# Performance work log

Hardware: AMD Instinct MI355X
Metric: run time of the kernel (lower is better)

The kernel has to match this reference:

```python
import jax, jax.numpy as jnp
import numpy as np

EPS = 2.220446049250313e-16  # sys.float_info.epsilon
TEMP = 0.01

def maxpool2(x):
    b, c, h, w = x.shape
    return x.reshape(b, c, h // 2, 2, w // 2, 2).max(axis=(3, 5))

def conv1x1(x, w, b):
    # x: [B,C,H,W], w: [O,C], b: [O]
    return jnp.einsum('bchw,oc->bohw', x, w) + b[None, :, None, None]

def unfold3(x):
    # F.unfold(kernel_size=3, padding=1) -> [B, C*9, H*W], channel-major ordering
    b, c, h, w = x.shape
    xp = jnp.pad(x, ((0, 0), (0, 0), (1, 1), (1, 1)))
    patches = jnp.stack([xp[:, :, i:i + h, j:j + w] for i in range(3) for j in range(3)], axis=2)  # [b,c,9,h,w]
    return patches.reshape(b, c * 9, h * w)

def center_norm(t):
    # mean-center and L2-normalize over the patch-feature dim (dim=1)
    t = t - t.mean(axis=1, keepdims=True)
    return t / (jnp.linalg.norm(t, axis=1, keepdims=True) + EPS)

def setup_inputs() -> dict:
    key = jax.random.key(0)
    ks = jax.random.split(key, 12)
    B, C, H, W = 4, 256, 64, 64
    inp = {
        'block_fea': jax.random.normal(ks[0], (B, C, H, W), jnp.float32),
        'spp_input': jax.random.normal(ks[1], (B, C, H, W), jnp.float32),
        'click_map': jax.random.uniform(ks[2], (B, 2, H * 8, W * 8), jnp.float32),
        # click feature pyramid convs (1x1)
        'w1': jax.random.normal(ks[3], (64, 2), jnp.float32) * 0.1,
        'b1': jnp.zeros((64,), jnp.float32),
        'w2': jax.random.normal(ks[4], (128, 64), jnp.float32) * 0.05,
        'b2': jnp.zeros((128,), jnp.float32),
        'w3': jax.random.normal(ks[5], (256, 128), jnp.float32) * 0.05,
        'b3': jnp.zeros((256,), jnp.float32),
        # final cat conv: 512 -> 256
        'wc': jax.random.normal(ks[6], (256, 512), jnp.float32) * 0.03,
        'bc': jnp.zeros((256,), jnp.float32),
    }
    return inp

def reference(block_fea, spp_input, click_map, w1, b1, w2, b2, w3, b3, wc, bc):
    B, C, H, W = block_fea.shape
    HW = H * W
    # click feature: MaxPool-Conv x3 (2ch -> 64 -> 128 -> 256), spatial /8
    cf = conv1x1(maxpool2(click_map), w1, b1)
    cf = conv1x1(maxpool2(cf), w2, b2)
    cf = conv1x1(maxpool2(cf), w3, b3)  # [B,256,H,W]
    # get_corre: unfold + mean-center + L2-normalize (cosine similarity over 3x3 patches)
    theta = center_norm(unfold3(block_fea))  # [B, C*9, HW]
    # spp_input is already (H,W): bilinear interpolate to same size is identity
    phi = center_norm(unfold3(spp_input))    # [B, C*9, HW]
    f = jnp.einsum('bcm,bcn->bmn', theta, phi) / TEMP  # [B, HW, HW]
    f_div_C = jax.nn.softmax(f, axis=-1)
    # propagate: click_fea already (H,W) -> identity interpolate
    ref = cf.reshape(B, C, HW)
    y = jnp.einsum('bmn,bcn->bcm', f_div_C, ref).reshape(B, C, H, W)
    # upsample to (H,W) is identity; concat + 1x1 conv
    out = conv1x1(jnp.concatenate([block_fea, y], axis=1), wc, bc)
    return out
```

## Files before the change

kernel.cpp:

```cpp
#include <hip/hip_runtime.h>
#include <math.h>

#define EPSF 2.220446049250313e-16f

typedef short bf16x8 __attribute__((ext_vector_type(8)));
typedef float f32x4 __attribute__((ext_vector_type(4)));

static __device__ __forceinline__ unsigned short f2bf(float x) {
  union { float f; unsigned u; } v; v.f = x;
  unsigned r = v.u + 0x7fffu + ((v.u >> 16) & 1u);
  return (unsigned short)(r >> 16);
}

__global__ __launch_bounds__(256) void k_zero(float* __restrict__ p) {
  const int t = blockIdx.x * 256 + threadIdx.x;
  float4 z = make_float4(0.f, 0.f, 0.f, 0.f);
  *reinterpret_cast<float4*>(&p[(size_t)t * 4]) = z;
}

__global__ __launch_bounds__(256) void k_tcast(const float* __restrict__ src0,
    unsigned short* __restrict__ dst0, int R, int C,
    size_t src_z, size_t dst_z, float* __restrict__ SA, float* __restrict__ QA) {
  __shared__ float ld[64][65];
  const float* src = src0 + blockIdx.z * src_z;
  unsigned short* dst = dst0 + blockIdx.z * dst_z;
  const int c0 = blockIdx.x * 64, r0 = blockIdx.y * 64;
  const int t = threadIdx.x;
  const int colr = t & 63, rowr = t >> 6;
  float s = 0.f, q = 0.f;
  #pragma unroll
  for (int i = 0; i < 16; ++i) {
    const int rl = rowr + i * 4;
    const float v = src[(size_t)(r0 + rl) * C + c0 + colr];
    ld[colr][rl] = v;
    s += v; q += v * v;
  }
  if (SA) {
    atomicAdd(&SA[blockIdx.z * 4096 + c0 + colr], s);
    atomicAdd(&QA[blockIdx.z * 4096 + c0 + colr], q);
  }
  __syncthreads();
  const int rl = t & 63, clb = t >> 6;
  #pragma unroll
  for (int i = 0; i < 16; ++i) {
    const int cl = clb + i * 4;
    dst[(size_t)(c0 + cl) * R + r0 + rl] = f2bf(ld[cl][rl]);
  }
}

__global__ __launch_bounds__(128) void k_pyr1(const float* __restrict__ click,
    const float* __restrict__ w1, const float* __restrict__ b1,
    const float* __restrict__ w2, const float* __restrict__ b2,
    float* __restrict__ cf2) {
  __shared__ float pool1[16][8];
  __shared__ float pooled64[16][64];
  const int b = blockIdx.y;
  const int pg = blockIdx.x;
  const int tid = threadIdx.x;
  {
    const int q = tid >> 3, s = (tid >> 1) & 3, c = tid & 1;
    const int p2 = pg * 16 + q;
    const int y2 = p2 >> 7, x2 = p2 & 127;
    const int sy = s >> 1, sx = s & 1;
    const int row = 4 * y2 + 2 * sy, col = 4 * x2 + 2 * sx;
    const float* base = click + (((size_t)(b * 2 + c)) * 512 + row) * 512 + col;
    pool1[q][s * 2 + c] = fmaxf(fmaxf(base[0], base[1]), fmaxf(base[512], base[513]));
  }
  __syncthreads();
  {
    const int c1 = tid & 63, qh = tid >> 6;
    const float wa = w1[c1 * 2], wb = w1[c1 * 2 + 1], bb = b1[c1];
    #pragma unroll
    for (int r = 0; r < 8; ++r) {
      const int q = qh * 8 + r;
      float v = -3.4e38f;
      #pragma unroll
      for (int s = 0; s < 4; ++s)
        v = fmaxf(v, bb + wa * pool1[q][s * 2] + wb * pool1[q][s * 2 + 1]);
      pooled64[q][c1] = v;
    }
  }
  __syncthreads();
  float acc[16];
  #pragma unroll
  for (int q = 0; q < 16; ++q) acc[q] = b2[tid];
  const float4* wrow = reinterpret_cast<const float4*>(w2 + tid * 64);
  #pragma unroll
  for (int k4 = 0; k4 < 16; ++k4) {
    const float4 w = wrow[k4];
    #pragma unroll
    for (int q = 0; q < 16; ++q) {
      const float4 p = *reinterpret_cast<const float4*>(&pooled64[q][k4 * 4]);
      acc[q] += w.x * p.x + w.y * p.y + w.z * p.z + w.w * p.w;
    }
  }
  #pragma unroll
  for (int q = 0; q < 16; ++q)
    cf2[((size_t)b * 16384 + pg * 16 + q) * 128 + tid] = acc[q];
}

__global__ __launch_bounds__(256) void k_pyr2(const float* __restrict__ cf2,
    const float* __restrict__ w3, const float* __restrict__ b3,
    float* __restrict__ cf3) {
  __shared__ float pooled[16][128];
  const int b = blockIdx.y;
  const int pb = blockIdx.x;
  const int tid = threadIdx.x;
  #pragma unroll
  for (int i = 0; i < 8; ++i) {
    const int idx = tid + 256 * i;
    const int q = idx >> 7, c = idx & 127;
    const int p = pb * 16 + q;
    const int y = p >> 6, x = p & 63;
    const size_t r0 = (size_t)b * 16384 + (2 * y) * 128 + 2 * x;
    const float* s0 = cf2 + r0 * 128 + c;
    pooled[q][c] = fmaxf(fmaxf(s0[0], s0[128]), fmaxf(s0[128 * 128], s0[128 * 129]));
  }
  __syncthreads();
  float acc[16];
  #pragma unroll
  for (int q = 0; q < 16; ++q) acc[q] = b3[tid];
  const float4* wrow = reinterpret_cast<const float4*>(w3 + tid * 128);
  #pragma unroll
  for (int k4 = 0; k4 < 32; ++k4) {
    const float4 w = wrow[k4];
    #pragma unroll
    for (int q = 0; q < 16; ++q) {
      const float4 p = *reinterpret_cast<const float4*>(&pooled[q][k4 * 4]);
      acc[q] += w.x * p.x + w.y * p.y + w.z * p.z + w.w * p.w;
    }
  }
  #pragma unroll
  for (int q = 0; q < 16; ++q)
    cf3[((size_t)b * 4096 + pb * 16 + q) * 256 + tid] = acc[q];
}

__global__ __launch_bounds__(256) void k_stats9(const float* __restrict__ SA,
    const float* __restrict__ QA, const float* __restrict__ SB, const float* __restrict__ QB,
    float* __restrict__ muA, float* __restrict__ invA,
    float* __restrict__ muB, float* __restrict__ invB) {
  const int b = blockIdx.y;
  const int m = blockIdx.x * 256 + threadIdx.x;
  const int y = m >> 6, x = m & 63;
  const int base = b * 4096;
  float sa = 0, qa = 0, sb = 0, qb = 0;
  #pragma unroll
  for (int dy = -1; dy <= 1; ++dy) {
    const int yy = y + dy;
    if ((unsigned)yy >= 64u) continue;
    #pragma unroll
    for (int dx = -1; dx <= 1; ++dx) {
      const int xx = x + dx;
      if ((unsigned)xx >= 64u) continue;
      const int idx = base + yy * 64 + xx;
      sa += SA[idx]; qa += QA[idx];
      sb += SB[idx]; qb += QB[idx];
    }
  }
  const float ma = sa * (1.f / 2304.f);
  const float mb = sb * (1.f / 2304.f);
  const float na = sqrtf(fmaxf(qa - 2304.f * ma * ma, 0.f));
  const float nb = sqrtf(fmaxf(qb - 2304.f * mb * mb, 0.f));
  muA[base + m] = ma;
  invA[base + m] = 1.f / (na + EPSF);
  muB[base + m] = mb;
  invB[base + m] = 1.f / (nb + EPSF);
}

#define ROWP 40
static __device__ __forceinline__ void stage_tile(const unsigned short* __restrict__ src,
    size_t srow, int r0, int k0, unsigned short* __restrict__ lds, int tid) {
  #pragma unroll
  for (int p = 0; p < 2; ++p) {
    const int idx = tid + p * 256;
    const int m = idx >> 2, q = idx & 3;
    const bf16x8 v = *reinterpret_cast<const bf16x8*>(src + (size_t)(r0 + m) * srow + k0 + q * 8);
    *reinterpret_cast<bf16x8*>(lds + m * ROWP + q * 8) = v;
  }
}

static __device__ __forceinline__ bf16x8 frag(const unsigned short* __restrict__ lds,
                                              int row, int q) {
  return *reinterpret_cast<const bf16x8*>(lds + row * ROWP + q * 8);
}

__global__ __launch_bounds__(256) void k_gemm_g(const unsigned short* __restrict__ At,
    const unsigned short* __restrict__ Bt, float* __restrict__ G) {
  __shared__ unsigned short As[128 * ROWP];
  __shared__ unsigned short Bs[128 * ROWP];
  const int tid = threadIdx.x;
  const int lin = blockIdx.y * 32 + blockIdx.x;
  const int nlin = ((lin & 7) << 7) | (lin >> 3);
  const int m0 = (nlin >> 5) * 128, n0 = (nlin & 31) * 128;
  const int l = tid & 63, w = tid >> 6;
  const int wr = w >> 1, wc = w & 1;
  const int q = l >> 4, lr = l & 15;
  f32x4 acc[4][4];
  #pragma unroll
  for (int i = 0; i < 4; ++i)
    #pragma unroll
    for (int j = 0; j < 4; ++j)
      acc[i][j] = f32x4{0.f, 0.f, 0.f, 0.f};
  for (int k0 = 0; k0 < 256; k0 += 32) {
    stage_tile(At, 256, m0, k0, As, tid);
    stage_tile(Bt, 256, n0, k0, Bs, tid);
    __syncthreads();
    bf16x8 a[4], bvv[4];
    #pragma unroll
    for (int i = 0; i < 4; ++i) a[i] = frag(As, wr * 64 + i * 16 + lr, q);
    #pragma unroll
    for (int j = 0; j < 4; ++j) bvv[j] = frag(Bs, wc * 64 + j * 16 + lr, q);
    #pragma unroll
    for (int i = 0; i < 4; ++i)
      #pragma unroll
      for (int j = 0; j < 4; ++j)
        acc[i][j] = __builtin_amdgcn_mfma_f32_16x16x32_bf16(a[i], bvv[j], acc[i][j], 0, 0, 0);
    __syncthreads();
  }
  const int rb = 4 * q;
  #pragma unroll
  for (int i = 0; i < 4; ++i)
    #pragma unroll
    for (int j = 0; j < 4; ++j) {
      const size_t base = (size_t)(m0 + wr * 64 + i * 16 + rb) * 4096 + n0 + wc * 64 + j * 16 + lr;
      #pragma unroll
      for (int r = 0; r < 4; ++r)
        G[base + (size_t)r * 4096] = acc[i][j][r];
    }
}

__global__ __launch_bounds__(256) void k_fsoft(const float* __restrict__ G,
    const float* __restrict__ muA, const float* __restrict__ invA,
    const float* __restrict__ muB, const float* __restrict__ invB,
    unsigned short* __restrict__ P) {
  __shared__ float redm[4];
  __shared__ float reds[4];
  const int m = ((blockIdx.x & 7) << 9) | (blockIdx.x >> 3);
  const int tid = threadIdx.x;
  const int ym = m >> 6, xm = m & 63;
  const int xn = tid & 63, ty = tid >> 6;

  const float* base[9];
  bool xok[9];
  #pragma unroll
  for (int dy = -1; dy <= 1; ++dy) {
    #pragma unroll
    for (int dx = -1; dx <= 1; ++dx) {
      const int g = (dy + 1) * 3 + (dx + 1);
      const bool rv = ((unsigned)(ym + dy) < 64u) && ((unsigned)(xm + dx) < 64u);
      const int d = dy * 64 + dx;
      base[g] = rv ? (G + (size_t)(m + d) * 4096 + d) : G;
      xok[g] = rv && ((unsigned)(xn + dx) < 64u);
    }
  }

  float acc[16];
  #pragma unroll
  for (int u = 0; u < 16; ++u) acc[u] = 0.f;

  #pragma unroll
  for (int uc = 0; uc < 4; ++uc) {
    float v[36];
    #pragma unroll
    for (int g = 0; g < 9; ++g) {
      #pragma unroll
      for (int r = 0; r < 4; ++r) {
        const int u = uc * 4 + r;
        v[g * 4 + r] = base[g][u * 256 + tid];
      }
    }
    #pragma unroll
    for (int g = 0; g < 9; ++g) {
      const int dy = g / 3 - 1;
      #pragma unroll
      for (int r = 0; r < 4; ++r) {
        const int u = uc * 4 + r;
        const bool ok = xok[g] && ((unsigned)(4 * u + ty + dy) < 64u);
        acc[u] += ok ? v[g * 4 + r] : 0.f;
      }
    }
  }

  const float s1 = 2304.f * muA[m];
  const float ia100 = invA[m] * 100.f;
  float mx = -3.4e38f;
  #pragma unroll
  for (int u = 0; u < 16; ++u) {
    const int n = tid + u * 256;
    const float lg = (acc[u] - s1 * muB[n]) * (ia100 * invB[n]);
    acc[u] = lg;
    mx = fmaxf(mx, lg);
  }
  #pragma unroll
  for (int off = 32; off; off >>= 1) mx = fmaxf(mx, __shfl_xor(mx, off));
  const int wave = tid >> 6, lane = tid & 63;
  if (lane == 0) redm[wave] = mx;
  __syncthreads();
  mx = fmaxf(fmaxf(redm[0], redm[1]), fmaxf(redm[2], redm[3]));
  float s = 0.f;
  #pragma unroll
  for (int u = 0; u < 16; ++u) {
    acc[u] = __expf(acc[u] - mx);
    s += acc[u];
  }
  #pragma unroll
  for (int off = 32; off; off >>= 1) s += __shfl_xor(s, off);
  if (lane == 0) reds[wave] = s;
  __syncthreads();
  s = reds[0] + reds[1] + reds[2] + reds[3];
  const float inv = 1.f / s;
  unsigned short* row = P + (size_t)m * 4096;
  #pragma unroll
  for (int u = 0; u < 16; ++u)
    row[tid + u * 256] = f2bf(acc[u] * inv);
}

__global__ __launch_bounds__(256) void k_pv(const unsigned short* __restrict__ CFt,
    const unsigned short* __restrict__ P, float* __restrict__ Y) {
  __shared__ unsigned short As[128 * ROWP];
  __shared__ unsigned short Bs[128 * ROWP];
  const int tid = threadIdx.x;
  const int c0 = blockIdx.y * 128, mb0 = blockIdx.x * 128;
  const int kbase = blockIdx.z * 512;
  const int l = tid & 63, w = tid >> 6;
  const int wr = w >> 1, wc = w & 1;
  const int q = l >> 4, lr = l & 15;
  f32x4 acc[4][4];
  #pragma unroll
  for (int i = 0; i < 4; ++i)
    #pragma unroll
    for (int j = 0; j < 4; ++j)
      acc[i][j] = f32x4{0.f, 0.f, 0.f, 0.f};
  for (int ks = 0; ks < 512; ks += 32) {
    const int k0 = kbase + ks;
    stage_tile(CFt, 4096, c0, k0, As, tid);
    stage_tile(P, 4096, mb0, k0, Bs, tid);
    __syncthreads();
    bf16x8 a[4], bvv[4];
    #pragma unroll
    for (int i = 0; i < 4; ++i) a[i] = frag(As, wr * 64 + i * 16 + lr, q);
    #pragma unroll
    for (int j = 0; j < 4; ++j) bvv[j] = frag(Bs, wc * 64 + j * 16 + lr, q);
    #pragma unroll
    for (int i = 0; i < 4; ++i)
      #pragma unroll
      for (int j = 0; j < 4; ++j)
        acc[i][j] = __builtin_amdgcn_mfma_f32_16x16x32_bf16(a[i], bvv[j], acc[i][j], 0, 0, 0);
    __syncthreads();
  }
  const int rb = 4 * q;
  #pragma unroll
  for (int i = 0; i < 4; ++i)
    #pragma unroll
    for (int j = 0; j < 4; ++j) {
      #pragma unroll
      for (int r = 0; r < 4; ++r) {
        const size_t o = (size_t)(c0 + wr * 64 + i * 16 + rb + r) * 4096 + mb0 + wc * 64 + j * 16 + lr;
        atomicAdd(&Y[o], acc[i][j][r]);
      }
    }
}

__global__ __launch_bounds__(256) void k_final(const float* __restrict__ WC,
    const float* __restrict__ bc, const float* __restrict__ BF,
    const float* __restrict__ Y, float* __restrict__ OUT) {
  __shared__ float As[16][68];
  __shared__ float Bs[16][64];
  const int b = blockIdx.z;
  const int tid = threadIdx.x;
  const int tx = tid & 15, ty = tid >> 4;
  const int o0 = blockIdx.y * 64, m0 = blockIdx.x * 64;
  float acc[4][4] = {};
  for (int k0 = 0; k0 < 512; k0 += 16) {
    #pragma unroll
    for (int t = 0; t < 4; ++t) {
      const int e = tid + t * 256;
      const int oo = e >> 4, kk = e & 15;
      As[kk][oo] = WC[(size_t)(o0 + oo) * 512 + k0 + kk];
    }
    #pragma unroll
    for (int t = 0; t < 4; ++t) {
      const int e = tid + t * 256;
      const int kk = e >> 6, col = e & 63;
      const int k = k0 + kk;
      const float* src = (k < 256)
          ? (BF + ((size_t)(b * 256 + k)) * 4096)
          : (Y + ((size_t)(b * 256 + (k - 256))) * 4096);
      Bs[kk][col] = src[m0 + col];
    }
    __syncthreads();
    #pragma unroll
    for (int k = 0; k < 16; ++k) {
      const float4 a4 = *reinterpret_cast<const float4*>(&As[k][ty * 4]);
      const float4 b4 = *reinterpret_cast<const float4*>(&Bs[k][tx * 4]);
      const float av[4] = {a4.x, a4.y, a4.z, a4.w};
      const float bv[4] = {b4.x, b4.y, b4.z, b4.w};
      #pragma unroll
      for (int i = 0; i < 4; ++i)
        #pragma unroll
        for (int j = 0; j < 4; ++j)
          acc[i][j] += av[i] * bv[j];
    }
    __syncthreads();
  }
  #pragma unroll
  for (int i = 0; i < 4; ++i) {
    const int o = o0 + ty * 4 + i;
    const float bias = bc[o];
    float4 v = make_float4(acc[i][0] + bias, acc[i][1] + bias,
                           acc[i][2] + bias, acc[i][3] + bias);
    *reinterpret_cast<float4*>(&OUT[((size_t)(b * 256 + o)) * 4096 + m0 + tx * 4]) = v;
  }
}

extern "C" void kernel_launch(void* const* d_in, const int* in_sizes, int n_in,
                              void* d_out, int out_size, void* d_ws, size_t ws_size,
                              hipStream_t stream) {
  const float* block_fea = (const float*)d_in[0];
  const float* spp       = (const float*)d_in[1];
  const float* click     = (const float*)d_in[2];
  const float* w1 = (const float*)d_in[3];
  const float* b1 = (const float*)d_in[4];
  const float* w2 = (const float*)d_in[5];
  const float* b2 = (const float*)d_in[6];
  const float* w3 = (const float*)d_in[7];
  const float* b3 = (const float*)d_in[8];
  const float* wc = (const float*)d_in[9];
  const float* bc = (const float*)d_in[10];
  float* out = (float*)d_out;

  float* ws = (float*)d_ws;
  const size_t M1 = 1024 * 1024;
  float* cf2  = ws;
  float* G    = ws + 256;
  unsigned short* Pb  = (unsigned short*)(ws + 17 * M1);
  unsigned short* At  = (unsigned short*)(ws + 25 * M1);
  unsigned short* Bt  = (unsigned short*)(ws + 27 * M1);
  unsigned short* CFt = (unsigned short*)(ws + 29 * M1);
  float* cf3  = ws + 31 * M1;
  float* Y    = ws + 35 * M1;
  float* SA   = ws + 39 * M1;
  float* QA   = SA + 16384;
  float* SB   = QA + 16384;
  float* QB   = SB + 16384;
  float* muA  = QB + 16384;
  float* invA = muA + 16384;
  float* muB  = invA + 16384;
  float* invB = muB + 16384;

  k_zero<<<dim3(4160), 256, 0, stream>>>(Y);
  k_pyr1<<<dim3(1024, 4), 128, 0, stream>>>(click, w1, b1, w2, b2, cf2);
  k_pyr2<<<dim3(256, 4), 256, 0, stream>>>(cf2, w3, b3, cf3);
  k_tcast<<<dim3(64, 4, 4), 256, 0, stream>>>(block_fea, At, 256, 4096,
                                              (size_t)256 * 4096, (size_t)4096 * 256, SA, QA);
  k_tcast<<<dim3(64, 4, 4), 256, 0, stream>>>(spp, Bt, 256, 4096,
                                              (size_t)256 * 4096, (size_t)4096 * 256, SB, QB);
  k_tcast<<<dim3(4, 64, 4), 256, 0, stream>>>(cf3, CFt, 4096, 256,
                                              (size_t)4096 * 256, (size_t)256 * 4096,
                                              (float*)nullptr, (float*)nullptr);
  k_stats9<<<dim3(16, 4), 256, 0, stream>>>(SA, QA, SB, QB, muA, invA, muB, invB);

  for (int b = 0; b < 4; ++b) {
    const unsigned short* Atb = At + (size_t)b * 4096 * 256;
    const unsigned short* Btb = Bt + (size_t)b * 4096 * 256;
    k_gemm_g<<<dim3(32, 32), 256, 0, stream>>>(Atb, Btb, G);
    k_fsoft<<<dim3(4096), 256, 0, stream>>>(G, muA + b * 4096, invA + b * 4096,
                                            muB + b * 4096, invB + b * 4096, Pb);
    k_pv<<<dim3(32, 2, 8), 256, 0, stream>>>(CFt + (size_t)b * 256 * 4096, Pb,
                                             Y + (size_t)b * 256 * 4096);
  }

  k_final<<<dim3(64, 4, 4), 256, 0, stream>>>(wc, bc, block_fea, Y, out);
}
```

Before: 625.1 us.

## Reassociate the final conv into the propagation GEMM and drop the fp32 final kernel

The final 1x1 conv is split over the concatenated input. The block_fea half becomes a bf16 MFMA GEMM that writes bias-initialised output. The click-feature half is applied to cf3 before propagation, so k_pv atomically accumulates straight into the output. This removes the scalar fp32 k_final GEMM, the large Y zeroing and the cf3 transpose, adding two small MFMA GEMMs and a weight split/cast kernel. The trade-off is extra bf16 rounding on block_fea, the weights and the pre-multiplied click features.

Result: faster. 574.8 us (-8.1%).

```diff
diff --git a/kernel.cpp b/kernel.cpp
--- a/kernel.cpp
+++ b/kernel.cpp
@@ -16,6 +16,15 @@
   const int t = blockIdx.x * 256 + threadIdx.x;
   float4 z = make_float4(0.f, 0.f, 0.f, 0.f);
   *reinterpret_cast<float4*>(&p[(size_t)t * 4]) = z;
+}
+
+__global__ __launch_bounds__(256) void k_wsplit(const float* __restrict__ wc,
+    unsigned short* __restrict__ wcLb, unsigned short* __restrict__ wcRb) {
+  const int idx = blockIdx.x * 256 + threadIdx.x;
+  const int o = idx >> 9, k = idx & 511;
+  const float v = wc[idx];
+  if (k < 256) wcLb[o * 256 + k] = f2bf(v);
+  else         wcRb[o * 256 + (k - 256)] = f2bf(v);
 }
 
 __global__ __launch_bounds__(256) void k_tcast(const float* __restrict__ src0,
@@ -101,7 +110,7 @@
 
 __global__ __launch_bounds__(256) void k_pyr2(const float* __restrict__ cf2,
     const float* __restrict__ w3, const float* __restrict__ b3,
-    float* __restrict__ cf3) {
+    unsigned short* __restrict__ cf3b) {
   __shared__ float pooled[16][128];
   const int b = blockIdx.y;
   const int pb = blockIdx.x;
@@ -132,7 +141,7 @@
   }
   #pragma unroll
   for (int q = 0; q < 16; ++q)
-    cf3[((size_t)b * 4096 + pb * 16 + q) * 256 + tid] = acc[q];
+    cf3b[((size_t)b * 4096 + pb * 16 + q) * 256 + tid] = f2bf(acc[q]);
 }
 
 __global__ __launch_bounds__(256) void k_stats9(const float* __restrict__ SA,
@@ -229,6 +238,100 @@
     }
 }
 
+__global__ __launch_bounds__(256) void k_gemm_cf2(const unsigned short* __restrict__ wcRb,
+    const unsigned short* __restrict__ cf3b, unsigned short* __restrict__ CF2t) {
+  __shared__ unsigned short As[128 * ROWP];
+  __shared__ unsigned short Bs[128 * ROWP];
+  const int b = blockIdx.z;
+  const int tid = threadIdx.x;
+  const int o0 = blockIdx.y * 128, n0 = blockIdx.x * 128;
+  const unsigned short* Bb = cf3b + (size_t)b * 4096 * 256;
+  unsigned short* outb = CF2t + (size_t)b * 256 * 4096;
+  const int l = tid & 63, w = tid >> 6;
+  const int wr = w >> 1, wcol = w & 1;
+  const int q = l >> 4, lr = l & 15;
+  f32x4 acc[4][4];
+  #pragma unroll
+  for (int i = 0; i < 4; ++i)
+    #pragma unroll
+    for (int j = 0; j < 4; ++j)
+      acc[i][j] = f32x4{0.f, 0.f, 0.f, 0.f};
+  for (int k0 = 0; k0 < 256; k0 += 32) {
+    stage_tile(wcRb, 256, o0, k0, As, tid);
+    stage_tile(Bb, 256, n0, k0, Bs, tid);
+    __syncthreads();
+    bf16x8 a[4], bvv[4];
+    #pragma unroll
+    for (int i = 0; i < 4; ++i) a[i] = frag(As, wr * 64 + i * 16 + lr, q);
+    #pragma unroll
+    for (int j = 0; j < 4; ++j) bvv[j] = frag(Bs, wcol * 64 + j * 16 + lr, q);
+    #pragma unroll
+    for (int i = 0; i < 4; ++i)
+      #pragma unroll
+      for (int j = 0; j < 4; ++j)
+        acc[i][j] = __builtin_amdgcn_mfma_f32_16x16x32_bf16(a[i], bvv[j], acc[i][j], 0, 0, 0);
+    __syncthreads();
+  }
+  const int rb = 4 * q;
+  #pragma unroll
+  for (int i = 0; i < 4; ++i)
+    #pragma unroll
+    for (int j = 0; j < 4; ++j) {
+      const size_t base = (size_t)(o0 + wr * 64 + i * 16 + rb) * 4096 + n0 + wcol * 64 + j * 16 + lr;
+      #pragma unroll
+      for (int r = 0; r < 4; ++r)
+        outb[base + (size_t)r * 4096] = f2bf(acc[i][j][r]);
+    }
+}
+
+__global__ __launch_bounds__(256) void k_gemm_oinit(const unsigned short* __restrict__ wcLb,
+    const unsigned short* __restrict__ At, const float* __restrict__ bc,
+    float* __restrict__ OUT) {
+  __shared__ unsigned short As[128 * ROWP];
+  __shared__ unsigned short Bs[128 * ROWP];
+  const int b = blockIdx.z;
+  const int tid = threadIdx.x;
+  const int o0 = blockIdx.y * 128, m0 = blockIdx.x * 128;
+  const unsigned short* Bb = At + (size_t)b * 4096 * 256;
+  float* outb = OUT + (size_t)b * 256 * 4096;
+  const int l = tid & 63, w = tid >> 6;
+  const int wr = w >> 1, wcol = w & 1;
+  const int q = l >> 4, lr = l & 15;
+  f32x4 acc[4][4];
+  #pragma unroll
+  for (int i = 0; i < 4; ++i)
+    #pragma unroll
+    for (int j = 0; j < 4; ++j)
+      acc[i][j] = f32x4{0.f, 0.f, 0.f, 0.f};
+  for (int k0 = 0; k0 < 256; k0 += 32) {
+    stage_tile(wcLb, 256, o0, k0, As, tid);
+    stage_tile(Bb, 256, m0, k0, Bs, tid);
+    __syncthreads();
+    bf16x8 a[4], bvv[4];
+    #pragma unroll
+    for (int i = 0; i < 4; ++i) a[i] = frag(As, wr * 64 + i * 16 + lr, q);
+    #pragma unroll
+    for (int j = 0; j < 4; ++j) bvv[j] = frag(Bs, wcol * 64 + j * 16 + lr, q);
+    #pragma unroll
+    for (int i = 0; i < 4; ++i)
+      #pragma unroll
+      for (int j = 0; j < 4; ++j)
+        acc[i][j] = __builtin_amdgcn_mfma_f32_16x16x32_bf16(a[i], bvv[j], acc[i][j], 0, 0, 0);
+    __syncthreads();
+  }
+  const int rb = 4 * q;
+  #pragma unroll
+  for (int i = 0; i < 4; ++i)
+    #pragma unroll
+    for (int j = 0; j < 4; ++j) {
+      #pragma unroll
+      for (int r = 0; r < 4; ++r) {
+        const int o = o0 + wr * 64 + i * 16 + rb + r;
+        outb[(size_t)o * 4096 + m0 + wcol * 64 + j * 16 + lr] = acc[i][j][r] + bc[o];
+      }
+    }
+}
+
 __global__ __launch_bounds__(256) void k_fsoft(const float* __restrict__ G,
     const float* __restrict__ muA, const float* __restrict__ invA,
     const float* __restrict__ muB, const float* __restrict__ invB,
@@ -315,8 +418,8 @@
     row[tid + u * 256] = f2bf(acc[u] * inv);
 }
 
-__global__ __launch_bounds__(256) void k_pv(const unsigned short* __restrict__ CFt,
-    const unsigned short* __restrict__ P, float* __restrict__ Y) {
+__global__ __launch_bounds__(256) void k_pv(const unsigned short* __restrict__ CF2t,
+    const unsigned short* __restrict__ P, float* __restrict__ OUT) {
   __shared__ unsigned short As[128 * ROWP];
   __shared__ unsigned short Bs[128 * ROWP];
   const int tid = threadIdx.x;
@@ -333,7 +436,7 @@
       acc[i][j] = f32x4{0.f, 0.f, 0.f, 0.f};
   for (int ks = 0; ks < 512; ks += 32) {
     const int k0 = kbase + ks;
-    stage_tile(CFt, 4096, c0, k0, As, tid);
+    stage_tile(CF2t, 4096, c0, k0, As, tid);
     stage_tile(P, 4096, mb0, k0, Bs, tid);
     __syncthreads();
     bf16x8 a[4], bvv[4];
@@ -356,61 +459,9 @@
       #pragma unroll
       for (int r = 0; r < 4; ++r) {
         const size_t o = (size_t)(c0 + wr * 64 + i * 16 + rb + r) * 4096 + mb0 + wc * 64 + j * 16 + lr;
-        atomicAdd(&Y[o], acc[i][j][r]);
+        atomicAdd(&OUT[o], acc[i][j][r]);
       }
     }
-}
-
-__global__ __launch_bounds__(256) void k_final(const float* __restrict__ WC,
-    const float* __restrict__ bc, const float* __restrict__ BF,
-    const float* __restrict__ Y, float* __restrict__ OUT) {
-  __shared__ float As[16][68];
-  __shared__ float Bs[16][64];
-  const int b = blockIdx.z;
-  const int tid = threadIdx.x;
-  const int tx = tid & 15, ty = tid >> 4;
-  const int o0 = blockIdx.y * 64, m0 = blockIdx.x * 64;
-  float acc[4][4] = {};
-  for (int k0 = 0; k0 < 512; k0 += 16) {
-    #pragma unroll
-    for (int t = 0; t < 4; ++t) {
-      const int e = tid + t * 256;
-      const int oo = e >> 4, kk = e & 15;
-      As[kk][oo] = WC[(size_t)(o0 + oo) * 512 + k0 + kk];
-    }
-    #pragma unroll
-    for (int t = 0; t < 4; ++t) {
-      const int e = tid + t * 256;
-      const int kk = e >> 6, col = e & 63;
-      const int k = k0 + kk;
-      const float* src = (k < 256)
-          ? (BF + ((size_t)(b * 256 + k)) * 4096)
-          : (Y + ((size_t)(b * 256 + (k - 256))) * 4096);
-      Bs[kk][col] = src[m0 + col];
-    }
-    __syncthreads();
-    #pragma unroll
-    for (int k = 0; k < 16; ++k) {
-      const float4 a4 = *reinterpret_cast<const float4*>(&As[k][ty * 4]);
-      const float4 b4 = *reinterpret_cast<const float4*>(&Bs[k][tx * 4]);
-      const float av[4] = {a4.x, a4.y, a4.z, a4.w};
-      const float bv[4] = {b4.x, b4.y, b4.z, b4.w};
-      #pragma unroll
-      for (int i = 0; i < 4; ++i)
-        #pragma unroll
-        for (int j = 0; j < 4; ++j)
-          acc[i][j] += av[i] * bv[j];
-    }
-    __syncthreads();
-  }
-  #pragma unroll
-  for (int i = 0; i < 4; ++i) {
-    const int o = o0 + ty * 4 + i;
-    const float bias = bc[o];
-    float4 v = make_float4(acc[i][0] + bias, acc[i][1] + bias,
-                           acc[i][2] + bias, acc[i][3] + bias);
-    *reinterpret_cast<float4*>(&OUT[((size_t)(b * 256 + o)) * 4096 + m0 + tx * 4]) = v;
-  }
 }
 
 extern "C" void kernel_launch(void* const* d_in, const int* in_sizes, int n_in,
@@ -433,13 +484,14 @@
   const size_t M1 = 1024 * 1024;
   float* cf2  = ws;
   float* G    = ws + 256;
-  unsigned short* Pb  = (unsigned short*)(ws + 17 * M1);
-  unsigned short* At  = (unsigned short*)(ws + 25 * M1);
-  unsigned short* Bt  = (unsigned short*)(ws + 27 * M1);
-  unsigned short* CFt = (unsigned short*)(ws + 29 * M1);
-  float* cf3  = ws + 31 * M1;
-  float* Y    = ws + 35 * M1;
-  float* SA   = ws + 39 * M1;
+  unsigned short* Pb   = (unsigned short*)(ws + 17 * M1);
+  unsigned short* At   = (unsigned short*)(ws + 25 * M1);
+  unsigned short* Bt   = (unsigned short*)(ws + 27 * M1);
+  unsigned short* CF3b = (unsigned short*)(ws + 29 * M1);
+  unsigned short* CF2t = (unsigned short*)(ws + 31 * M1);
+  unsigned short* wcLb = (unsigned short*)(ws + 35 * M1);
+  unsigned short* wcRb = wcLb + 65536;
+  float* SA   = ws + 36 * M1;
   float* QA   = SA + 16384;
   float* SB   = QA + 16384;
   float* QB   = SB + 16384;
@@ -448,17 +500,17 @@
   float* muB  = invA + 16384;
   float* invB = muB + 16384;
 
-  k_zero<<<dim3(4160), 256, 0, stream>>>(Y);
+  k_zero<<<dim3(64), 256, 0, stream>>>(SA);
+  k_wsplit<<<dim3(512), 256, 0, stream>>>(wc, wcLb, wcRb);
   k_pyr1<<<dim3(1024, 4), 128, 0, stream>>>(click, w1, b1, w2, b2, cf2);
-  k_pyr2<<<dim3(256, 4), 256, 0, stream>>>(cf2, w3, b3, cf3);
+  k_pyr2<<<dim3(256, 4), 256, 0, stream>>>(cf2, w3, b3, CF3b);
   k_tcast<<<dim3(64, 4, 4), 256, 0, stream>>>(block_fea, At, 256, 4096,
                                               (size_t)256 * 4096, (size_t)4096 * 256, SA, QA);
   k_tcast<<<dim3(64, 4, 4), 256, 0, stream>>>(spp, Bt, 256, 4096,
                                               (size_t)256 * 4096, (size_t)4096 * 256, SB, QB);
-  k_tcast<<<dim3(4, 64, 4), 256, 0, stream>>>(cf3, CFt, 4096, 256,
-                                              (size_t)4096 * 256, (size_t)256 * 4096,
-                                              (float*)nullptr, (float*)nullptr);
   k_stats9<<<dim3(16, 4), 256, 0, stream>>>(SA, QA, SB, QB, muA, invA, muB, invB);
+  k_gemm_cf2<<<dim3(32, 2, 4), 256, 0, stream>>>(wcRb, CF3b, CF2t);
+  k_gemm_oinit<<<dim3(32, 2, 4), 256, 0, stream>>>(wcLb, At, bc, out);
 
   for (int b = 0; b < 4; ++b) {
     const unsigned short* Atb = At + (size_t)b * 4096 * 256;
@@ -466,9 +518,7 @@
     k_gemm_g<<<dim3(32, 32), 256, 0, stream>>>(Atb, Btb, G);
     k_fsoft<<<dim3(4096), 256, 0, stream>>>(G, muA + b * 4096, invA + b * 4096,
                                             muB + b * 4096, invB + b * 4096, Pb);
-    k_pv<<<dim3(32, 2, 8), 256, 0, stream>>>(CFt + (size_t)b * 256 * 4096, Pb,
-                                             Y + (size_t)b * 256 * 4096);
-  }
-
-  k_final<<<dim3(64, 4, 4), 256, 0, stream>>>(wc, bc, block_fea, Y, out);
-}
+    k_pv<<<dim3(32, 2, 8), 256, 0, stream>>>(CF2t + (size_t)b * 256 * 4096, Pb,
+                                             out + (size_t)b * 256 * 4096);
+  }
+}
```
